# Optimization experiments

Hardware: AMD Instinct MI355X
Metric: run time of the kernel (lower is better)

## Reference

```python
import jax, jax.numpy as jnp
import numpy as np

DIM = 512
DK = 128
G = 256            # group_size
HID = int(DIM * 4.0)
NUM_BUCKETS = 32
MAX_DIST = 128
REL_SCALE = G ** 0.5
LN_EPS = 1e-5


def _rel_pos_bucket(rel_pos):
    # T5RelativePositionBias._relative_position_bucket, non-causal
    nb = NUM_BUCKETS // 2          # 16
    n = -rel_pos
    ret = (n < 0).astype(jnp.int32) * nb
    n = jnp.abs(n)
    max_exact = nb // 2            # 8
    is_small = n < max_exact
    n_safe = jnp.maximum(n, 1).astype(jnp.float32)
    val_if_large = max_exact + (
        jnp.log(n_safe / max_exact) / np.log(MAX_DIST / max_exact) * (nb - max_exact)
    ).astype(jnp.int32)
    val_if_large = jnp.minimum(val_if_large, nb - 1)
    return ret + jnp.where(is_small, n, val_if_large)


def _laplace_attn(x):
    mu = np.sqrt(0.5)
    std = np.sqrt(0.25 * np.pi)
    return 0.5 * (1.0 + jax.lax.erf((x - mu) / (std * np.sqrt(2.0))))


def setup_inputs() -> dict:
    key = jax.random.key(0)
    ks = jax.random.split(key, 8)
    b, n = 8, 4096
    w = 0.02
    return {
        "x": jax.random.normal(ks[0], (b, n, DIM), dtype=jnp.float32),
        "mask": jnp.ones((b, n), dtype=bool),
        "ln_gamma": jnp.ones((DIM,), jnp.float32),
        "ln_beta": jnp.zeros((DIM,), jnp.float32),
        "W_hidden": jax.random.normal(ks[1], (DIM, 2 * HID), jnp.float32) * w,
        "b_hidden": jnp.zeros((2 * HID,), jnp.float32),
        "W_qk": jax.random.normal(ks[2], (DIM, DK), jnp.float32) * w,
        "b_qk": jnp.zeros((DK,), jnp.float32),
        "os_gamma": 1.0 + jax.random.normal(ks[3], (4, DK), jnp.float32) * w,
        "os_beta": jnp.zeros((4, DK), jnp.float32),
        "rel_bias": jax.random.normal(ks[4], (NUM_BUCKETS,), jnp.float32) * w,
        "W_out": jax.random.normal(ks[5], (HID, DIM), jnp.float32) * w,
        "b_out": jnp.zeros((DIM,), jnp.float32),
    }


def reference(x, mask, ln_gamma, ln_beta, W_hidden, b_hidden, W_qk, b_qk,
              os_gamma, os_beta, rel_bias, W_out, b_out):
    b, n, d = x.shape
    g = G
    # pre-norm (LayerNorm)
    mu = jnp.mean(x, axis=-1, keepdims=True)
    var = jnp.var(x, axis=-1, keepdims=True)
    normed = (x - mu) * jax.lax.rsqrt(var + LN_EPS) * ln_gamma + ln_beta
    # gated hidden (v, gate) and qk with SiLU
    h = jax.nn.silu(normed @ W_hidden + b_hidden)        # [b, n, 2*HID]
    v, gate = jnp.split(h, 2, axis=-1)                   # [b, n, HID] each
    qk = jax.nn.silu(normed @ W_qk + b_qk)               # [b, n, DK]
    # OffsetScale into 4 heads: quad_q, lin_q, quad_k, lin_k
    qk4 = qk[..., None, :] * os_gamma + os_beta          # [b, n, 4, DK]
    quad_q, lin_q, quad_k, lin_k = (qk4[..., i, :] for i in range(4))
    # zero out masked linear-attention keys
    lin_k = jnp.where(mask[..., None], lin_k, 0.0)
    # group along sequence (n is a multiple of g -> no padding)
    ng = n // g
    grp = lambda t: t.reshape(b, ng, g, t.shape[-1])
    qq, qkk, lq, lk, vg = map(grp, (quad_q, quad_k, lin_q, lin_k, v))
    mg = mask.reshape(b, ng, 1, g)                       # [b, g, 1, j]
    # quadratic attention within groups, laplace kernel + T5 rel-pos bias
    sim = jnp.einsum('bgid,bgjd->bgij', qq, qkk) / g
    pos = jnp.arange(g)
    rel = pos[None, :] - pos[:, None]                    # [i, j] = k_pos - q_pos
    bias = rel_bias[_rel_pos_bucket(rel)] * REL_SCALE
    attn = _laplace_attn(sim + bias)
    attn = jnp.where(mg, attn, 0.0)
    quad_out = jnp.einsum('bgij,bgjd->bgid', attn, vg)
    # linear (global) attention, groups reduced (reduce_group_non_causal_attn=True)
    lin_kv = jnp.einsum('bgnd,bgne->bde', lk, vg) / n
    lin_out = jnp.einsum('bgnd,bde->bgne', lq, lin_kv)
    # gate, project out, residual
    out = gate * (quad_out + lin_out).reshape(b, n, -1)
    return out @ W_out + b_out + x
```

## Files before the change

kernel.cpp:

```cpp
#include <hip/hip_runtime.h>
#include <math.h>


typedef __attribute__((ext_vector_type(8))) short short8;
typedef __attribute__((ext_vector_type(4))) float f32x4;

#define CSTR 134

union alignas(16) SMem {
  struct { short A[3][4096]; short B[3][4096]; } ab;
  short ct[128 * CSTR];
  float sf[64 * 132];
};

__device__ __forceinline__ unsigned short f2bf(float f) {
  unsigned int u = __float_as_uint(f);
  unsigned int r = (u + 0x7FFFu + ((u >> 16) & 1u)) >> 16;
  return (unsigned short)r;
}
__device__ __forceinline__ float bf2f(unsigned short s) {
  return __uint_as_float(((unsigned int)s) << 16);
}
__device__ __forceinline__ unsigned int cvt_pk_bf16(float lo, float hi) {
  unsigned int r;
  asm("v_cvt_pk_bf16_f32 %0, %1, %2" : "=v"(r) : "v"(lo), "v"(hi));
  return r;
}
__device__ __forceinline__ f32x4 mfma16(short8 a, short8 b, f32x4 c) {
  return __builtin_amdgcn_mfma_f32_16x16x32_bf16(a, b, c, 0, 0, 0);
}
__device__ __forceinline__ float silu(float z) {
  float e = __builtin_amdgcn_exp2f(-1.44269504089f * z);
  return z * __builtin_amdgcn_rcpf(1.0f + e);
}

__device__ __forceinline__ void dma16(const short* g, short* l) {
  __builtin_amdgcn_global_load_lds(
      (const __attribute__((address_space(1))) unsigned int*)(const void*)g,
      (__attribute__((address_space(3))) unsigned int*)(void*)l, 16, 0, 0);
}

__device__ __forceinline__ void gemm_core(
    const short* __restrict__ A, long lda,
    const short* __restrict__ B, long ldb,
    int K, short (*As)[4096], short (*Bs)[4096], f32x4 (&acc)[4][4])
{
  const int tid = threadIdx.x, lane = tid & 63, wave = tid >> 6;
  const int wm = (wave >> 1) * 64, wn = (wave & 1) * 64;
  const int q = lane >> 4, l15 = lane & 15;
  const long ga = (long)(lane >> 2) * lda + (lane & 3) * 8;
  const long gb = (long)(lane >> 2) * ldb + (lane & 3) * 8;
  const int r0 = wave * 32;
  const int nk = K >> 5;
  __syncthreads();
#pragma unroll
  for (int t = 0; t < 2; ++t)
#pragma unroll
    for (int j = 0; j < 2; ++j) {
      dma16(A + t*32 + (long)(r0 + j*16) * lda + ga, As[t] + (r0 + j*16) * 32);
      dma16(B + t*32 + (long)(r0 + j*16) * ldb + gb, Bs[t] + (r0 + j*16) * 32);
    }
  for (int kt = 0; kt < nk; ++kt) {
    if (kt < nk - 1) asm volatile("s_waitcnt vmcnt(4) lgkmcnt(0)" ::: "memory");
    else             asm volatile("s_waitcnt vmcnt(0) lgkmcnt(0)" ::: "memory");
    __builtin_amdgcn_s_barrier();
    __builtin_amdgcn_sched_barrier(0);
    if (kt + 2 < nk) {
      const int nb = (kt + 2) % 3;
      const short* Ak = A + (kt + 2) * 32;
      const short* Bk = B + (kt + 2) * 32;
#pragma unroll
      for (int j = 0; j < 2; ++j) {
        dma16(Ak + (long)(r0 + j*16) * lda + ga, As[nb] + (r0 + j*16) * 32);
        dma16(Bk + (long)(r0 + j*16) * ldb + gb, Bs[nb] + (r0 + j*16) * 32);
      }
    }
    const int cur = kt % 3;
    short8 af[4], bfr[4];
#pragma unroll
    for (int mt = 0; mt < 4; ++mt)
      af[mt] = *(const short8*)(const void*)&As[cur][(wm + mt*16 + l15) * 32 + q*8];
#pragma unroll
    for (int nt = 0; nt < 4; ++nt)
      bfr[nt] = *(const short8*)(const void*)&Bs[cur][(wn + nt*16 + l15) * 32 + q*8];
#pragma unroll
    for (int mt = 0; mt < 4; ++mt)
#pragma unroll
      for (int nt = 0; nt < 4; ++nt)
        acc[mt][nt] = mfma16(af[mt], bfr[nt], acc[mt][nt]);
  }
}

#define EPI_VARS \
  const int lane = threadIdx.x & 63; const int wave = threadIdx.x >> 6; \
  const int wm = (wave >> 1) * 64; const int wn = (wave & 1) * 64;      \
  const int q = lane >> 4; const int l15 = lane & 15;

#define DECL_ACC f32x4 acc[4][4]; \
  _Pragma("unroll") for (int mt_ = 0; mt_ < 4; ++mt_) \
  _Pragma("unroll") for (int nt_ = 0; nt_ < 4; ++nt_) { f32x4 z_ = {0.f,0.f,0.f,0.f}; acc[mt_][nt_] = z_; }

__device__ __forceinline__ void stage_tile(short* ct, const f32x4 (&acc)[4][4], bool transpose) {
  EPI_VARS;
  __syncthreads();
  if (transpose) {
#pragma unroll
    for (int mt = 0; mt < 4; ++mt)
#pragma unroll
      for (int nt = 0; nt < 4; ++nt) {
        const int row0 = wm + mt*16 + q*4;
        const int col = wn + nt*16 + l15;
#pragma unroll
        for (int r2 = 0; r2 < 2; ++r2) {
          unsigned int pk = cvt_pk_bf16(acc[mt][nt][2*r2], acc[mt][nt][2*r2+1]);
          *(unsigned int*)(void*)&ct[col * CSTR + row0 + 2*r2] = pk;
        }
      }
  } else {
#pragma unroll
    for (int mt = 0; mt < 4; ++mt)
#pragma unroll
      for (int nt = 0; nt < 4; ++nt) {
        const int row0 = wm + mt*16 + q*4;
        const int col = wn + nt*16 + l15;
#pragma unroll
        for (int r2 = 0; r2 < 2; ++r2) {
          unsigned int pk = cvt_pk_bf16(acc[mt][nt][2*r2], acc[mt][nt][2*r2+1]);
          ct[(row0 + 2*r2)     * CSTR + col] = (short)(pk & 0xFFFFu);
          ct[(row0 + 2*r2 + 1) * CSTR + col] = (short)(pk >> 16);
        }
      }
  }
  __syncthreads();
}

__global__ __launch_bounds__(256) void k_transpose_bf16(
    const float* __restrict__ src, short* __restrict__ dst, int R, int C)
{
  __shared__ float tile[32][33];
  const int tx = threadIdx.x & 31, ty = threadIdx.x >> 5;
  const long c0 = (long)blockIdx.x * 32, r0 = (long)blockIdx.y * 32;
  for (int i = ty; i < 32; i += 8)
    tile[i][tx] = src[(r0 + i) * C + c0 + tx];
  __syncthreads();
  for (int i = ty; i < 32; i += 8)
    dst[(c0 + i) * R + r0 + tx] = (short)f2bf(tile[tx][i]);
}

__global__ __launch_bounds__(256) void k_bias(const float* __restrict__ rel_bias,
                                              float* __restrict__ biasTab)
{
  const int i = blockIdx.x, j = threadIdx.x;
  int nn = i - j;
  int ret = (nn < 0) ? 16 : 0;
  int na = (nn < 0) ? -nn : nn;
  int v;
  if (na < 8) v = na;
  else {
    double t = log((double)na / 8.0) / log(16.0) * 8.0;
    v = 8 + (int)t;
    if (v > 15) v = 15;
  }
  biasTab[i * 256 + j] = rel_bias[ret + v] * 16.0f;
}

__global__ __launch_bounds__(256) void k_ln(const float* __restrict__ x,
    const float* __restrict__ g, const float* __restrict__ b, short* __restrict__ normed)
{
  const int wave = threadIdx.x >> 6, lane = threadIdx.x & 63;
  const long row = (long)blockIdx.x * 4 + wave;
  const float* xr = x + row * 512 + lane * 8;
  float4 a = *(const float4*)(const void*)xr;
  float4 c = *(const float4*)(const void*)(xr + 4);
  float s  = a.x + a.y + a.z + a.w + c.x + c.y + c.z + c.w;
  float sq = a.x*a.x + a.y*a.y + a.z*a.z + a.w*a.w + c.x*c.x + c.y*c.y + c.z*c.z + c.w*c.w;
  for (int m = 32; m >= 1; m >>= 1) { s += __shfl_xor(s, m); sq += __shfl_xor(sq, m); }
  const float mu  = s * (1.0f / 512.0f);
  const float var = sq * (1.0f / 512.0f) - mu * mu;
  const float inv = rsqrtf(var + 1e-5f);
  float4 g0 = *(const float4*)(const void*)(g + lane*8);
  float4 g1 = *(const float4*)(const void*)(g + lane*8 + 4);
  float4 b0 = *(const float4*)(const void*)(b + lane*8);
  float4 b1 = *(const float4*)(const void*)(b + lane*8 + 4);
  int4 pk;
  pk.x = (int)cvt_pk_bf16((a.x - mu) * inv * g0.x + b0.x, (a.y - mu) * inv * g0.y + b0.y);
  pk.y = (int)cvt_pk_bf16((a.z - mu) * inv * g0.z + b0.z, (a.w - mu) * inv * g0.w + b0.w);
  pk.z = (int)cvt_pk_bf16((c.x - mu) * inv * g1.x + b1.x, (c.y - mu) * inv * g1.y + b1.y);
  pk.w = (int)cvt_pk_bf16((c.z - mu) * inv * g1.z + b1.z, (c.w - mu) * inv * g1.w + b1.w);
  *(int4*)(void*)(normed + row * 512 + lane * 8) = pk;
}

__global__ __launch_bounds__(256) void k_gemm1(const short* __restrict__ normed,
    const short* __restrict__ WhT, const float* __restrict__ bh,
    short* __restrict__ vT_blk, short* __restrict__ gate)
{
  __shared__ SMem sm;
  DECL_ACC;
  const long m0 = (long)blockIdx.x * 128;
  const long n0 = (long)blockIdx.y * 128;
  gemm_core(normed + m0 * 512, 512, WhT + n0 * 512, 512, 512, sm.ab.A, sm.ab.B, acc);
  EPI_VARS;
  const bool isv = (blockIdx.y < 16);
#pragma unroll
  for (int mt = 0; mt < 4; ++mt)
#pragma unroll
    for (int nt = 0; nt < 4; ++nt) {
      const int n = (int)n0 + wn + nt*16 + l15;
      const float bbv = bh[n];
#pragma unroll
      for (int r = 0; r < 4; ++r) acc[mt][nt][r] = silu(acc[mt][nt][r] + bbv);
    }
  stage_tile(sm.ct, acc, isv);
  const int tid = threadIdx.x;
  if (isv) {
    const long g = m0 >> 8;
    const int tl0 = (int)(m0 & 255);
#pragma unroll
    for (int p = 0; p < 8; ++p) {
      const int idx = p * 256 + tid;
      const int row = idx >> 4, col = (idx & 15) * 8;
      int4 v = *(const int4*)(const void*)(sm.ct + row * CSTR + col);
      *(int4*)(void*)(vT_blk + (g * 2048 + n0 + row) * 256 + tl0 + col) = v;
    }
  } else {
#pragma unroll
    for (int p = 0; p < 8; ++p) {
      const int idx = p * 256 + tid;
      const int row = idx >> 4, col = (idx & 15) * 8;
      int4 v = *(const int4*)(const void*)(sm.ct + row * CSTR + col);
      *(int4*)(void*)(gate + (m0 + row) * 2048 + (n0 - 2048) + col) = v;
    }
  }
}

__global__ __launch_bounds__(256) void k_qkos(const short* __restrict__ normed,
    const short* __restrict__ WqkT, const float* __restrict__ bqk,
    const float* __restrict__ osg, const float* __restrict__ osb,
    short* __restrict__ qq, short* __restrict__ lq_, short* __restrict__ qkk,
    short* __restrict__ lkT_blk)
{
  __shared__ SMem sm;
  DECL_ACC;
  const long m0 = (long)blockIdx.x * 128;
  gemm_core(normed + m0 * 512, 512, WqkT, 512, 512, sm.ab.A, sm.ab.B, acc);
  EPI_VARS;
#pragma unroll
  for (int mt = 0; mt < 4; ++mt)
#pragma unroll
    for (int nt = 0; nt < 4; ++nt) {
      const int n = wn + nt*16 + l15;
      const float bbv = bqk[n];
#pragma unroll
      for (int r = 0; r < 4; ++r) acc[mt][nt][r] = silu(acc[mt][nt][r] + bbv);
    }
  stage_tile(sm.ct, acc, false);
  const int tid = threadIdx.x;
  const int col = (tid & 15) * 8;
  float ga[3][8], bb[3][8];
#pragma unroll
  for (int h = 0; h < 3; ++h) {
    float4 x0 = *(const float4*)(const void*)(osg + h*128 + col);
    float4 x1 = *(const float4*)(const void*)(osg + h*128 + col + 4);
    float4 y0 = *(const float4*)(const void*)(osb + h*128 + col);
    float4 y1 = *(const float4*)(const void*)(osb + h*128 + col + 4);
    ga[h][0]=x0.x; ga[h][1]=x0.y; ga[h][2]=x0.z; ga[h][3]=x0.w;
    ga[h][4]=x1.x; ga[h][5]=x1.y; ga[h][6]=x1.z; ga[h][7]=x1.w;
    bb[h][0]=y0.x; bb[h][1]=y0.y; bb[h][2]=y0.z; bb[h][3]=y0.w;
    bb[h][4]=y1.x; bb[h][5]=y1.y; bb[h][6]=y1.z; bb[h][7]=y1.w;
  }
  short* dsts[3] = {qq, lq_, qkk};
#pragma unroll
  for (int p = 0; p < 8; ++p) {
    const int idx = p * 256 + tid;
    const int row = idx >> 4;
    int4 v = *(const int4*)(const void*)(sm.ct + row * CSTR + col);
    const unsigned short* vs = (const unsigned short*)&v;
#pragma unroll
    for (int h = 0; h < 3; ++h) {
      int4 o; unsigned int* op = (unsigned int*)&o;
#pragma unroll
      for (int jj = 0; jj < 4; ++jj)
        op[jj] = cvt_pk_bf16(bf2f(vs[2*jj])   * ga[h][2*jj]   + bb[h][2*jj],
                             bf2f(vs[2*jj+1]) * ga[h][2*jj+1] + bb[h][2*jj+1]);
      *(int4*)(void*)(dsts[h] + (m0 + row) * 128 + col) = o;
    }
  }
#pragma unroll
  for (int nt = 0; nt < 4; ++nt) {
    const int n = wn + nt*16 + l15;
    const float g3 = osg[3*128 + n], b3 = osb[3*128 + n];
#pragma unroll
    for (int mt = 0; mt < 4; ++mt)
#pragma unroll
      for (int r = 0; r < 4; ++r) acc[mt][nt][r] = acc[mt][nt][r] * g3 + b3;
  }
  stage_tile(sm.ct, acc, true);
  const long g = m0 >> 8;
  const int t0 = (int)(m0 & 255);
#pragma unroll
  for (int p = 0; p < 8; ++p) {
    const int idx = p * 256 + tid;
    const int row = idx >> 4, col2 = (idx & 15) * 8;
    int4 v = *(const int4*)(const void*)(sm.ct + row * CSTR + col2);
    *(int4*)(void*)(lkT_blk + (g * 128 + row) * 256 + t0 + col2) = v;
  }
}

__global__ __launch_bounds__(256) void k_mid(const short* __restrict__ qq,
    const short* __restrict__ qkk, const float* __restrict__ biasTab,
    short* __restrict__ attnO,
    const short* __restrict__ vT_blk, const short* __restrict__ lkT_blk,
    float* __restrict__ partial, int KS, int gpk, int nAttn, int ngrp)
{
  __shared__ SMem sm;
  DECL_ACC;
  const int bx = blockIdx.x;
  if (bx < nAttn) {
    const int g = bx % ngrp, rem = bx / ngrp;
    const int im = rem & 1, jn = rem >> 1;
    gemm_core(qq  + (long)(g*256 + im*128) * 128, 128,
              qkk + (long)(g*256 + jn*128) * 128, 128, 128, sm.ab.A, sm.ab.B, acc);
    EPI_VARS;
#pragma unroll
    for (int mt = 0; mt < 4; ++mt)
#pragma unroll
      for (int nt = 0; nt < 4; ++nt) {
        const int j = jn*128 + wn + nt*16 + l15;
#pragma unroll
        for (int r = 0; r < 4; ++r) {
          const int i = im*128 + wm + mt*16 + q*4 + r;
          const float sim = acc[mt][nt][r] * 0.00390625f + biasTab[i * 256 + j];
          acc[mt][nt][r] = 0.5f * (1.0f + erff((sim - 0.70710678119f) * 0.79788456080f));
        }
      }
    stage_tile(sm.ct, acc, false);
    const int tid = threadIdx.x;
#pragma unroll
    for (int p = 0; p < 8; ++p) {
      const int idx = p * 256 + tid;
      const int row = idx >> 4, col = (idx & 15) * 8;
      int4 v = *(const int4*)(const void*)(sm.ct + row * CSTR + col);
      *(int4*)(void*)(attnO + (long)g * 65536 + (long)(im*128 + row) * 256 + jn*128 + col) = v;
    }
  } else {
    const int idx2 = bx - nAttn;
    const int b = idx2 % gpk;
    const int me = (idx2 / gpk) & 15;
    const int ks = idx2 / (gpk * 16);
    for (int gi = 0; gi < gpk; ++gi) {
      const long g = (long)b * 16 + (long)ks * gpk + gi;
      gemm_core(vT_blk + (g * 2048 + me * 128) * 256, 256,
                lkT_blk + g * 128 * 256, 256, 256, sm.ab.A, sm.ab.B, acc);
    }
    EPI_VARS;
    float* slice = partial + ((long)(b * KS + ks)) * 262144;
#pragma unroll
    for (int mt = 0; mt < 4; ++mt)
#pragma unroll
      for (int nt = 0; nt < 4; ++nt) {
        const int d = wn + nt*16 + l15;
#pragma unroll
        for (int r = 0; r < 4; ++r) {
          const int e = me*128 + wm + mt*16 + q*4 + r;
          slice[(long)e * 128 + d] = acc[mt][nt][r];
        }
      }
  }
}

__global__ __launch_bounds__(256) void k_quadfused(const short* __restrict__ attn,
    const short* __restrict__ vT_blk, const short* __restrict__ linkv16,
    const short* __restrict__ lq_, short* __restrict__ gate)
{
  __shared__ SMem sm;
  DECL_ACC;
  const int g = blockIdx.x, im = blockIdx.y, ie = blockIdx.z;
  const int b = g >> 4;
  const long t0 = (long)g * 256 + im * 128;
  const long e0 = (long)ie * 128;
  gemm_core(attn + (long)g * 65536 + (long)im * 128 * 256, 256,
            vT_blk + ((long)g * 2048 + e0) * 256, 256, 256, sm.ab.A, sm.ab.B, acc);
  gemm_core(lq_ + t0 * 128, 128,
            linkv16 + (long)b * 262144 + e0 * 128, 128, 128, sm.ab.A, sm.ab.B, acc);
  stage_tile(sm.ct, acc, false);
  const int tid = threadIdx.x;
#pragma unroll
  for (int p = 0; p < 8; ++p) {
    const int idx = p * 256 + tid;
    const int row = idx >> 4, col = (idx & 15) * 8;
    int4 cv = *(const int4*)(const void*)(sm.ct + row * CSTR + col);
    int4 gv = *(const int4*)(const void*)(gate + (t0 + row) * 2048 + e0 + col);
    const unsigned short* cs = (const unsigned short*)&cv;
    const unsigned short* gs = (const unsigned short*)&gv;
    int4 ov; unsigned int* op = (unsigned int*)&ov;
#pragma unroll
    for (int jj = 0; jj < 4; ++jj)
      op[jj] = cvt_pk_bf16(bf2f(gs[2*jj])   * bf2f(cs[2*jj]),
                           bf2f(gs[2*jj+1]) * bf2f(cs[2*jj+1]));
    *(int4*)(void*)(gate + (t0 + row) * 2048 + e0 + col) = ov;
  }
}

__global__ __launch_bounds__(256) void k_lkred(const float* __restrict__ partial,
    short* __restrict__ linkv16, int KS)
{
  const long i2 = ((long)blockIdx.x * 256 + threadIdx.x) * 2;
  const long b = i2 >> 18;
  const long within = i2 & 262143;
  const float* p = partial + b * KS * 262144 + within;
  float s0 = 0.f, s1 = 0.f;
  for (int ks = 0; ks < KS; ++ks) {
    float2 v = *(const float2*)(const void*)&p[(long)ks * 262144];
    s0 += v.x; s1 += v.y;
  }
  *(unsigned int*)(void*)&linkv16[i2] =
      cvt_pk_bf16(s0 * (1.0f / 4096.0f), s1 * (1.0f / 4096.0f));
}

__global__ __launch_bounds__(256) void k_out(const short* __restrict__ gate,
    const short* __restrict__ WoutT, const float* __restrict__ bo,
    const float* __restrict__ x, float* __restrict__ out)
{
  __shared__ SMem sm;
  DECL_ACC;
  const long m0 = (long)blockIdx.x * 128;
  const long n0 = (long)blockIdx.y * 128;
  gemm_core(gate + m0 * 2048, 2048, WoutT + n0 * 2048, 2048, 2048, sm.ab.A, sm.ab.B, acc);
  EPI_VARS;
  const int tid = threadIdx.x;
#pragma unroll
  for (int h = 0; h < 2; ++h) {
    __syncthreads();
    if ((wm >> 6) == h) {
#pragma unroll
      for (int mt = 0; mt < 4; ++mt)
#pragma unroll
        for (int nt = 0; nt < 4; ++nt)
#pragma unroll
          for (int r = 0; r < 4; ++r)
            sm.sf[(mt*16 + q*4 + r) * 132 + wn + nt*16 + l15] = acc[mt][nt][r];
    }
    __syncthreads();
#pragma unroll
    for (int p = 0; p < 8; ++p) {
      const int idx = p * 256 + tid;
      const int row = idx >> 5;
      const int c4 = (idx & 31) * 4;
      const long gm = m0 + h*64 + row;
      float4 a = *(const float4*)(const void*)&sm.sf[row * 132 + c4];
      float4 xv = *(const float4*)(const void*)(x + gm * 512 + n0 + c4);
      float4 b4 = *(const float4*)(const void*)(bo + n0 + c4);
      float4 o;
      o.x = a.x + b4.x + xv.x;
      o.y = a.y + b4.y + xv.y;
      o.z = a.z + b4.z + xv.z;
      o.w = a.w + b4.w + xv.w;
      *(float4*)(void*)(out + gm * 512 + n0 + c4) = o;
    }
  }
}

extern "C" void kernel_launch(void* const* d_in, const int* in_sizes, int n_in,
                              void* d_out, int out_size, void* d_ws, size_t ws_size,
                              hipStream_t stream) {
  (void)in_sizes; (void)n_in; (void)out_size;
  const float* x    = (const float*)d_in[0];
  const float* lng  = (const float*)d_in[2];
  const float* lnb  = (const float*)d_in[3];
  const float* Wh   = (const float*)d_in[4];
  const float* bh   = (const float*)d_in[5];
  const float* Wqk  = (const float*)d_in[6];
  const float* bqk  = (const float*)d_in[7];
  const float* osg  = (const float*)d_in[8];
  const float* osb  = (const float*)d_in[9];
  const float* relb = (const float*)d_in[10];
  const float* Wout = (const float*)d_in[11];
  const float* bo   = (const float*)d_in[12];
  float* out = (float*)d_out;

  auto bytesFor = [](int cb) -> size_t {
    long Tc = (long)cb * 4096;
    size_t s = 0;
    auto add = [&](size_t b) { s += (b + 255) & ~(size_t)255; };
    add(4096L*512*2); add(128L*512*2); add(512L*2048*2); add(256L*256*4);
    add(Tc*512*2);
    add(2048L*Tc*2);
    add(Tc*2048*2);
    add(Tc*128*2); add(Tc*128*2); add(Tc*128*2);
    add(128L*Tc*2);
    add((Tc/256)*65536L*2);
    add(16L*262144*4);
    add((long)cb*262144*2);
    return s;
  };
  int CB = 8;
  while (CB > 1 && bytesFor(CB) > ws_size) CB >>= 1;
  const long Tc = (long)CB * 4096;
  const int KS = 16 / CB;
  const int gpk = CB;

  char* ws = (char*)d_ws;
  size_t off = 0;
  auto alloc = [&](size_t bytes) -> void* {
    void* p = ws + off;
    off = (off + bytes + 255) & ~(size_t)255;
    return p;
  };
  short* WhT     = (short*)alloc(4096L * 512 * 2);
  short* WqkT    = (short*)alloc(128L * 512 * 2);
  short* WoutT   = (short*)alloc(512L * 2048 * 2);
  float* biasTab = (float*)alloc(256L * 256 * 4);
  short* normed  = (short*)alloc(Tc * 512 * 2);
  short* vT_blk  = (short*)alloc(2048L * Tc * 2);
  short* gate    = (short*)alloc(Tc * 2048 * 2);
  short* qq      = (short*)alloc(Tc * 128 * 2);
  short* lq_     = (short*)alloc(Tc * 128 * 2);
  short* qkk     = (short*)alloc(Tc * 128 * 2);
  short* lkT_blk = (short*)alloc(128L * Tc * 2);
  short* attn    = (short*)alloc((Tc/256) * 65536L * 2);
  float* partial = (float*)alloc(16L * 262144 * 4);
  short* linkv16 = (short*)alloc((long)CB * 262144 * 2);

  k_transpose_bf16<<<dim3(4096/32, 512/32), 256, 0, stream>>>(Wh, WhT, 512, 4096);
  k_transpose_bf16<<<dim3(128/32, 512/32),  256, 0, stream>>>(Wqk, WqkT, 512, 128);
  k_transpose_bf16<<<dim3(512/32, 2048/32), 256, 0, stream>>>(Wout, WoutT, 2048, 512);
  k_bias<<<256, 256, 0, stream>>>(relb, biasTab);

  const int nChunks = 8 / CB;
  const int ngrp = (int)(Tc / 256);
  const int nAttn = ngrp * 4;
  const int nLinkv = CB * 16 * KS;
  for (int c = 0; c < nChunks; ++c) {
    const long t0 = (long)c * Tc;
    const float* xc = x + t0 * 512;
    float* outc = out + t0 * 512;
    k_ln<<<(int)(Tc/4), 256, 0, stream>>>(xc, lng, lnb, normed);
    k_gemm1<<<dim3((int)(Tc/128), 32), 256, 0, stream>>>(normed, WhT, bh, vT_blk, gate);
    k_qkos<<<(int)(Tc/128), 256, 0, stream>>>(normed, WqkT, bqk, osg, osb, qq, lq_, qkk, lkT_blk);
    k_mid<<<nAttn + nLinkv, 256, 0, stream>>>(qq, qkk, biasTab, attn,
        vT_blk, lkT_blk, partial, KS, gpk, nAttn, ngrp);
    k_lkred<<<(int)(CB * 512), 256, 0, stream>>>(partial, linkv16, KS);
    k_quadfused<<<dim3((int)(Tc/256), 2, 16), 256, 0, stream>>>(attn, vT_blk, linkv16, lq_, gate);
    k_out<<<dim3((int)(Tc/128), 4), 256, 0, stream>>>(gate, WoutT, bo, xc, outc);
  }
}
```

Baseline: 608.4 us.

## Widen gemm1 tiles to 256x128 with 512-thread blocks sharing B tiles

The hidden-projection GEMM now uses 256-row by 128-column tiles computed by 8 waves per block, with a new wide GEMM core that loads twice as many A rows per stage while the B tile is shared. This halves the number of B (weight) tile loads per output and halves the block count. The epilogue stages the two 128-row halves through shared memory in turn to write vT and gate. The cost is larger shared memory per block, possibly lower occupancy, and extra barriers in the epilogue.

Result: slower. 675.4 us (+11.0%).

```diff
diff --git a/kernel.cpp b/kernel.cpp
--- a/kernel.cpp
+++ b/kernel.cpp
@@ -11,6 +11,11 @@
   struct { short A[3][4096]; short B[3][4096]; } ab;
   short ct[128 * CSTR];
   float sf[64 * 132];
+};
+
+union alignas(16) SMemW {
+  struct { short A[3][8192]; short B[3][4096]; } ab;
+  short ct[128 * CSTR];
 };
 
 __device__ __forceinline__ unsigned short f2bf(float f) {
@@ -74,6 +79,57 @@
         dma16(Ak + (long)(r0 + j*16) * lda + ga, As[nb] + (r0 + j*16) * 32);
         dma16(Bk + (long)(r0 + j*16) * ldb + gb, Bs[nb] + (r0 + j*16) * 32);
       }
+    }
+    const int cur = kt % 3;
+    short8 af[4], bfr[4];
+#pragma unroll
+    for (int mt = 0; mt < 4; ++mt)
+      af[mt] = *(const short8*)(const void*)&As[cur][(wm + mt*16 + l15) * 32 + q*8];
+#pragma unroll
+    for (int nt = 0; nt < 4; ++nt)
+      bfr[nt] = *(const short8*)(const void*)&Bs[cur][(wn + nt*16 + l15) * 32 + q*8];
+#pragma unroll
+    for (int mt = 0; mt < 4; ++mt)
+#pragma unroll
+      for (int nt = 0; nt < 4; ++nt)
+        acc[mt][nt] = mfma16(af[mt], bfr[nt], acc[mt][nt]);
+  }
+}
+
+__device__ __forceinline__ void gemm_core_wide(
+    const short* __restrict__ A, long lda,
+    const short* __restrict__ B, long ldb,
+    int K, short (*As)[8192], short (*Bs)[4096], f32x4 (&acc)[4][4])
+{
+  const int tid = threadIdx.x, lane = tid & 63, wave = tid >> 6;
+  const int wm = (wave >> 1) * 64, wn = (wave & 1) * 64;
+  const int q = lane >> 4, l15 = lane & 15;
+  const long ga = (long)(lane >> 2) * lda + (lane & 3) * 8;
+  const long gb = (long)(lane >> 2) * ldb + (lane & 3) * 8;
+  const int r0a = wave * 32;
+  const int r0b = wave * 16;
+  const int nk = K >> 5;
+  __syncthreads();
+#pragma unroll
+  for (int t = 0; t < 2; ++t) {
+#pragma unroll
+    for (int j = 0; j < 2; ++j)
+      dma16(A + t*32 + (long)(r0a + j*16) * lda + ga, As[t] + (r0a + j*16) * 32);
+    dma16(B + t*32 + (long)r0b * ldb + gb, Bs[t] + r0b * 32);
+  }
+  for (int kt = 0; kt < nk; ++kt) {
+    if (kt < nk - 1) asm volatile("s_waitcnt vmcnt(3) lgkmcnt(0)" ::: "memory");
+    else             asm volatile("s_waitcnt vmcnt(0) lgkmcnt(0)" ::: "memory");
+    __builtin_amdgcn_s_barrier();
+    __builtin_amdgcn_sched_barrier(0);
+    if (kt + 2 < nk) {
+      const int nb = (kt + 2) % 3;
+      const short* Ak = A + (kt + 2) * 32;
+      const short* Bk = B + (kt + 2) * 32;
+#pragma unroll
+      for (int j = 0; j < 2; ++j)
+        dma16(Ak + (long)(r0a + j*16) * lda + ga, As[nb] + (r0a + j*16) * 32);
+      dma16(Bk + (long)r0b * ldb + gb, Bs[nb] + r0b * 32);
     }
     const int cur = kt % 3;
     short8 af[4], bfr[4];
@@ -190,15 +246,15 @@
   *(int4*)(void*)(normed + row * 512 + lane * 8) = pk;
 }
 
-__global__ __launch_bounds__(256) void k_gemm1(const short* __restrict__ normed,
+__global__ __launch_bounds__(512) void k_gemm1(const short* __restrict__ normed,
     const short* __restrict__ WhT, const float* __restrict__ bh,
     short* __restrict__ vT_blk, short* __restrict__ gate)
 {
-  __shared__ SMem sm;
+  __shared__ SMemW sm;
   DECL_ACC;
-  const long m0 = (long)blockIdx.x * 128;
+  const long m0 = (long)blockIdx.x * 256;
   const long n0 = (long)blockIdx.y * 128;
-  gemm_core(normed + m0 * 512, 512, WhT + n0 * 512, 512, 512, sm.ab.A, sm.ab.B, acc);
+  gemm_core_wide(normed + m0 * 512, 512, WhT + n0 * 512, 512, 512, sm.ab.A, sm.ab.B, acc);
   EPI_VARS;
   const bool isv = (blockIdx.y < 16);
 #pragma unroll
@@ -210,25 +266,60 @@
 #pragma unroll
       for (int r = 0; r < 4; ++r) acc[mt][nt][r] = silu(acc[mt][nt][r] + bbv);
     }
-  stage_tile(sm.ct, acc, isv);
   const int tid = threadIdx.x;
-  if (isv) {
-    const long g = m0 >> 8;
-    const int tl0 = (int)(m0 & 255);
-#pragma unroll
-    for (int p = 0; p < 8; ++p) {
-      const int idx = p * 256 + tid;
-      const int row = idx >> 4, col = (idx & 15) * 8;
-      int4 v = *(const int4*)(const void*)(sm.ct + row * CSTR + col);
-      *(int4*)(void*)(vT_blk + (g * 2048 + n0 + row) * 256 + tl0 + col) = v;
-    }
-  } else {
-#pragma unroll
-    for (int p = 0; p < 8; ++p) {
-      const int idx = p * 256 + tid;
-      const int row = idx >> 4, col = (idx & 15) * 8;
-      int4 v = *(const int4*)(const void*)(sm.ct + row * CSTR + col);
-      *(int4*)(void*)(gate + (m0 + row) * 2048 + (n0 - 2048) + col) = v;
+  const long g = m0 >> 8;
+#pragma unroll
+  for (int h = 0; h < 2; ++h) {
+    __syncthreads();
+    if ((wave >> 2) == h) {
+      const int wml = wm & 127;
+      if (isv) {
+#pragma unroll
+        for (int nt = 0; nt < 4; ++nt) {
+          const int col = wn + nt*16 + l15;
+#pragma unroll
+          for (int mt = 0; mt < 4; ++mt) {
+            const int row0 = wml + mt*16 + q*4;
+#pragma unroll
+            for (int r2 = 0; r2 < 2; ++r2) {
+              unsigned int pk = cvt_pk_bf16(acc[mt][nt][2*r2], acc[mt][nt][2*r2+1]);
+              *(unsigned int*)(void*)&sm.ct[col * CSTR + row0 + 2*r2] = pk;
+            }
+          }
+        }
+      } else {
+#pragma unroll
+        for (int mt = 0; mt < 4; ++mt)
+#pragma unroll
+          for (int nt = 0; nt < 4; ++nt) {
+            const int row0 = wml + mt*16 + q*4;
+            const int col = wn + nt*16 + l15;
+#pragma unroll
+            for (int r2 = 0; r2 < 2; ++r2) {
+              unsigned int pk = cvt_pk_bf16(acc[mt][nt][2*r2], acc[mt][nt][2*r2+1]);
+              sm.ct[(row0 + 2*r2)     * CSTR + col] = (short)(pk & 0xFFFFu);
+              sm.ct[(row0 + 2*r2 + 1) * CSTR + col] = (short)(pk >> 16);
+            }
+          }
+      }
+    }
+    __syncthreads();
+    if (isv) {
+#pragma unroll
+      for (int p = 0; p < 4; ++p) {
+        const int idx = p * 512 + tid;
+        const int col = idx >> 4, r8 = (idx & 15) * 8;
+        int4 v = *(const int4*)(const void*)(sm.ct + col * CSTR + r8);
+        *(int4*)(void*)(vT_blk + (g * 2048 + n0 + col) * 256 + h*128 + r8) = v;
+      }
+    } else {
+#pragma unroll
+      for (int p = 0; p < 4; ++p) {
+        const int idx = p * 512 + tid;
+        const int row = idx >> 4, c8 = (idx & 15) * 8;
+        int4 v = *(const int4*)(const void*)(sm.ct + row * CSTR + c8);
+        *(int4*)(void*)(gate + (m0 + h*128 + row) * 2048 + (n0 - 2048) + c8) = v;
+      }
     }
   }
 }
@@ -535,7 +626,7 @@
     const float* xc = x + t0 * 512;
     float* outc = out + t0 * 512;
     k_ln<<<(int)(Tc/4), 256, 0, stream>>>(xc, lng, lnb, normed);
-    k_gemm1<<<dim3((int)(Tc/128), 32), 256, 0, stream>>>(normed, WhT, bh, vT_blk, gate);
+    k_gemm1<<<dim3((int)(Tc/256), 32), 512, 0, stream>>>(normed, WhT, bh, vT_blk, gate);
     k_qkos<<<(int)(Tc/128), 256, 0, stream>>>(normed, WqkT, bqk, osg, osb, qq, lq_, qkk, lkT_blk);
     k_mid<<<nAttn + nLinkv, 256, 0, stream>>>(qq, qkk, biasTab, attn,
         vT_blk, lkT_blk, partial, KS, gpk, nAttn, ngrp);
```
